# Kernel tuning notes

Measured on AMD Instinct MI355X. Metric: run time of the kernel, lower is better.

## Reference

```python
import jax, jax.numpy as jnp
import numpy as np

H = 256            # hidden_size
S = 4              # num_of_steps
B = 512            # reactions
N_MOLS = B * S     # 2048 molecules
ATOMS_PER_MOL = 32
N_ATOMS = N_MOLS * ATOMS_PER_MOL   # 65536
BONDS_PER_MOL = 64
N_BONDS = N_MOLS * BONDS_PER_MOL   # 131072 directed bonds (+1 pad row)
MAX_NB = 6
ATOM_FDIM = 133
BOND_FDIM = 147
DEPTH = 3
N_ITERS = 3  # Set2Set iterations


def setup_inputs() -> dict:
    key = jax.random.key(0)
    ks = jax.random.split(key, 20)
    def p(k, shape):
        return jax.random.normal(k, shape, jnp.float32) * 0.02
    inp = {}
    inp['f_atoms'] = jax.random.normal(ks[0], (N_ATOMS, ATOM_FDIM), jnp.float32)
    f_bonds = jax.random.normal(ks[1], (N_BONDS + 1, BOND_FDIM), jnp.float32)
    inp['f_bonds'] = f_bonds.at[0].set(0.0)  # chemprop zero pad row
    inp['a2b'] = jax.random.randint(ks[2], (N_ATOMS, MAX_NB), 0, N_BONDS + 1)
    inp['b2a'] = jax.random.randint(ks[3], (N_BONDS + 1,), 0, N_ATOMS)
    inp['b2revb'] = jax.random.randint(ks[4], (N_BONDS + 1,), 0, N_BONDS + 1)
    # MPN weights (bias=False for W_i/W_h as in args.bias default)
    inp['W_i'] = p(ks[5], (BOND_FDIM, H))
    inp['W_h'] = p(ks[6], (H, H))
    inp['W_o'] = p(ks[7], (ATOM_FDIM + H, H)); inp['b_o'] = jnp.zeros((H,), jnp.float32)
    # NNAttention over steps
    inp['W_nn0'] = p(ks[8], (2 * H, H));  inp['b_nn0'] = jnp.zeros((H,), jnp.float32)
    inp['W_nn0s'] = p(ks[9], (H, H));     inp['b_nn0s'] = jnp.zeros((H,), jnp.float32)
    inp['W_nn1'] = p(ks[10], (S * H, H)); inp['b_nn1'] = jnp.zeros((H,), jnp.float32)
    # node Set2Set (LSTM: input 2H -> hidden H) + condenser
    inp['lstm_n_Wih'] = p(ks[11], (4 * H, 2 * H))
    inp['lstm_n_Whh'] = p(ks[12], (4 * H, H))
    inp['lstm_n_b'] = jnp.zeros((4 * H,), jnp.float32)
    inp['node_cond_W'] = p(ks[13], (2 * H, H)); inp['node_cond_b'] = jnp.zeros((H,), jnp.float32)
    # graph (step) Set2Set + condenser
    inp['lstm_g_Wih'] = p(ks[14], (4 * H, 2 * H))
    inp['lstm_g_Whh'] = p(ks[15], (4 * H, H))
    inp['lstm_g_b'] = jnp.zeros((4 * H,), jnp.float32)
    inp['graph_cond_W'] = p(ks[16], (2 * H, H)); inp['graph_cond_b'] = jnp.zeros((H,), jnp.float32)
    return inp


def set2set(feat, Wih, Whh, b):
    # feat: [M, N, D]; LSTM n_layers=1, PyTorch gate order i,f,g,o
    M, N, D = feat.shape
    h = jnp.zeros((M, D), feat.dtype)
    c = jnp.zeros((M, D), feat.dtype)
    q_star = jnp.zeros((M, 2 * D), feat.dtype)
    for _ in range(N_ITERS):
        gates = q_star @ Wih.T + h @ Whh.T + b
        i, f, g, o = jnp.split(gates, 4, axis=-1)
        c = jax.nn.sigmoid(f) * c + jax.nn.sigmoid(i) * jnp.tanh(g)
        h = jax.nn.sigmoid(o) * jnp.tanh(c)
        q = h
        alpha = jax.nn.softmax(jnp.einsum('md,mnd->mn', q, feat), axis=1)
        readout = jnp.einsum('mn,mnd->md', alpha, feat)
        q_star = jnp.concatenate([q, readout], axis=-1)
    return q_star


def nn_attention(h, W0, b0, W0s, b0s, W1, b1):
    # vectorized form of the Attention module's s1/s2 double loop
    Bm, Sm, D = h.shape
    h1 = jnp.broadcast_to(h[:, :, None, :], (Bm, Sm, Sm, D))
    h2 = jnp.broadcast_to(h[:, None, :, :], (Bm, Sm, Sm, D))
    pair = jnp.concatenate([h1, h2], -1) @ W0 + b0          # [B,S,S,D] NN0(cat(h_s1,h_s2))
    self_o = h @ W0s + b0s                                   # [B,S,D]   NN0_self(h_s1)
    diag = jnp.eye(Sm, dtype=bool)[None, :, :, None]
    out = jnp.where(diag, self_o[:, :, None, :], pair)       # diagonal uses NN0_self
    return out.reshape(Bm, Sm, Sm * D) @ W1 + b1             # NN1 over s2-concat


def reference(f_atoms, f_bonds, a2b, b2a, b2revb, W_i, W_h, W_o, b_o,
              W_nn0, b_nn0, W_nn0s, b_nn0s, W_nn1, b_nn1,
              lstm_n_Wih, lstm_n_Whh, lstm_n_b, node_cond_W, node_cond_b,
              lstm_g_Wih, lstm_g_Whh, lstm_g_b, graph_cond_W, graph_cond_b):
    # --- bond message passing (chemprop, atom_messages=False) ---
    inp = f_bonds @ W_i                       # [NB+1, H], row 0 = 0 (no bias)
    message = jax.nn.relu(inp)
    message = message.at[0].set(0.0)          # keep pad row zero
    for _ in range(DEPTH - 1):
        a_message = message[a2b].sum(axis=1)          # gather+sum: [NA, H]
        msg = a_message[b2a] - message[b2revb]        # [NB+1, H]
        message = jax.nn.relu(inp + msg @ W_h)
        message = message.at[0].set(0.0)
    nei = message[a2b].sum(axis=1)                    # [NA, H]
    atom_h = jax.nn.relu(jnp.concatenate([f_atoms, nei], -1) @ W_o + b_o)
    # --- node readout: Set2Set per molecule + condenser ---
    feat = atom_h.reshape(N_MOLS, ATOMS_PER_MOL, H)
    mol = set2set(feat, lstm_n_Wih, lstm_n_Whh, lstm_n_b) @ node_cond_W + node_cond_b
    # --- step attention (NNAttention over num_of_steps) ---
    steps = mol.reshape(B, S, H)
    steps = nn_attention(steps, W_nn0, b_nn0, W_nn0s, b_nn0s, W_nn1, b_nn1)
    # --- step readout: Set2Set over steps + condenser ---
    out = set2set(steps, lstm_g_Wih, lstm_g_Whh, lstm_g_b) @ graph_cond_W + graph_cond_b
    return out  # [B, H]
```

## Files before the change

kernel.cpp:

```cpp
#include <hip/hip_runtime.h>
#include <math.h>

#define H 256
#define S_STEPS 4
#define B_RXN 512
#define N_MOLS 2048
#define ATOMS_PER_MOL 32
#define N_ATOMS 65536
#define N_BONDS 131072
#define NBP1 131073
#define MAX_NB 6
#define ATOM_FDIM 133
#define BOND_FDIM 147
#define DEPTH 3
#define N_ITERS 3

typedef unsigned short bf16u;
typedef __attribute__((ext_vector_type(8))) short short8v;
typedef __attribute__((ext_vector_type(4))) float f32x4;

__device__ __forceinline__ float b2f(bf16u u) {
    union { unsigned int i; float f; } c; c.i = ((unsigned int)u) << 16; return c.f;
}
__device__ __forceinline__ bf16u f2b(float f) {
    union { float f; unsigned int i; } c; c.f = f;
    unsigned int i = c.i;
    return (bf16u)((i + 0x7FFFu + ((i >> 16) & 1u)) >> 16);
}
__device__ __forceinline__ unsigned int relu2bf(unsigned int w) {
    unsigned int lo = w & 0xFFFFu, hi = w >> 16;
    if (lo & 0x8000u) lo = 0u;
    if (hi & 0x8000u) hi = 0u;
    return lo | (hi << 16);
}

template<int MODE, bool RELUA>
__global__ __launch_bounds__(512) void dense_gemm_k(
    const bf16u* __restrict__ A1,
    const bf16u* __restrict__ A2,
    const bf16u* __restrict__ WT,
    const float* __restrict__ bias,
    bf16u* __restrict__ outb,
    int M)
{
    constexpr int KP = (MODE == 0) ? 160 : ((MODE == 1) ? 256 : 416);
    __shared__ bf16u As[128][40];
    __shared__ bf16u Bs[256][40];

    const int tid = threadIdx.x;
    const int lane = tid & 63, w = tid >> 6;
    const int wr = w >> 2, wc = w & 3;
    const int m0 = blockIdx.x * 128;
    const int ar = tid >> 2, q8 = (tid & 3) * 8;
    const int br = tid >> 1, bh = (tid & 1) * 16;
    const int arow = m0 + ar;
    const bool rok = arow < M;
    const int lr = lane & 15, lk = (lane >> 4) * 8;
    const uint4 z4 = {0u, 0u, 0u, 0u};

    f32x4 acc[4][4];
    const f32x4 zf = {0.f, 0.f, 0.f, 0.f};
    #pragma unroll
    for (int i = 0; i < 4; ++i)
        #pragma unroll
        for (int j = 0; j < 4; ++j) acc[i][j] = zf;

    for (int k0 = 0; k0 < KP; k0 += 32) {
        const int kc = k0 + q8;
        uint4 va;
        if (MODE == 2) {
            va = (kc < 160) ? *(const uint4*)(A1 + (size_t)arow * 160 + kc)
                            : *(const uint4*)(A2 + (size_t)arow * 256 + (kc - 160));
        } else {
            constexpr int LDA = (MODE == 0) ? 160 : 256;
            va = rok ? *(const uint4*)(A1 + (size_t)arow * LDA + kc) : z4;
        }
        if (RELUA) {
            va.x = relu2bf(va.x); va.y = relu2bf(va.y);
            va.z = relu2bf(va.z); va.w = relu2bf(va.w);
        }
        *(uint4*)&As[ar][q8] = va;
        {
            const bf16u* bp = WT + (size_t)br * KP + k0 + bh;
            uint4 b0 = *(const uint4*)(bp);
            uint4 b1 = *(const uint4*)(bp + 8);
            *(uint4*)&Bs[br][bh] = b0;
            *(uint4*)&Bs[br][bh + 8] = b1;
        }
        __syncthreads();

        short8v a[4], b[4];
        #pragma unroll
        for (int mf = 0; mf < 4; ++mf)
            a[mf] = *(const short8v*)&As[wr * 64 + mf * 16 + lr][lk];
        #pragma unroll
        for (int nf = 0; nf < 4; ++nf)
            b[nf] = *(const short8v*)&Bs[wc * 64 + nf * 16 + lr][lk];
        #pragma unroll
        for (int mf = 0; mf < 4; ++mf)
            #pragma unroll
            for (int nf = 0; nf < 4; ++nf)
                acc[mf][nf] = __builtin_amdgcn_mfma_f32_16x16x32_bf16(
                    a[mf], b[nf], acc[mf][nf], 0, 0, 0);
        __syncthreads();
    }

    const int rbase = (lane >> 4) * 4;
    #pragma unroll
    for (int mf = 0; mf < 4; ++mf) {
        #pragma unroll
        for (int nf = 0; nf < 4; ++nf) {
            const int col = wc * 64 + nf * 16 + lr;
            #pragma unroll
            for (int r = 0; r < 4; ++r) {
                const int row = m0 + wr * 64 + mf * 16 + rbase + r;
                if (row >= M) continue;
                float v = acc[mf][nf][r];
                const size_t off = (size_t)row * H + col;
                if (MODE == 2) {
                    v += bias[col];
                    outb[off] = f2b(fmaxf(v, 0.f));
                } else {
                    outb[off] = f2b(v);
                }
            }
        }
    }
}

__global__ __launch_bounds__(256) void combine_k(
    const bf16u* __restrict__ inp, const bf16u* __restrict__ AP,
    const bf16u* __restrict__ MW,
    const int* __restrict__ b2a, const int* __restrict__ b2revb,
    bf16u* __restrict__ msg)
{
    int idx = blockIdx.x * 256 + threadIdx.x;
    if (idx >= NBP1 * 32) return;
    int b = idx >> 5, c = (idx & 31) * 8;
    bf16u* op = msg + (size_t)b * H + c;
    if (b == 0) {
        *(uint4*)op = make_uint4(0u, 0u, 0u, 0u);
        return;
    }
    int a = b2a[b], rb = b2revb[b];
    uint4 ui = *(const uint4*)(inp + (size_t)b * H + c);
    uint4 up = *(const uint4*)(AP + (size_t)a * H + c);
    uint4 um = *(const uint4*)(MW + (size_t)rb * H + c);
    uint4 o;
    unsigned int* pi = &ui.x; unsigned int* pp = &up.x;
    unsigned int* pm = &um.x; unsigned int* po = &o.x;
    #pragma unroll
    for (int t = 0; t < 4; ++t) {
        float lo = b2f((bf16u)(pi[t] & 0xFFFFu)) + b2f((bf16u)(pp[t] & 0xFFFFu))
                 - b2f((bf16u)(pm[t] & 0xFFFFu));
        float hi = b2f((bf16u)(pi[t] >> 16)) + b2f((bf16u)(pp[t] >> 16))
                 - b2f((bf16u)(pm[t] >> 16));
        lo = fmaxf(lo, 0.f); hi = fmaxf(hi, 0.f);
        po[t] = (unsigned int)f2b(lo) | ((unsigned int)f2b(hi) << 16);
    }
    *(uint4*)op = o;
}

template<bool BIAS>
__global__ __launch_bounds__(256) void lin64_k(
    const float* __restrict__ A1, int lda1, int KA1,
    const float* __restrict__ A2, int lda2,
    const bf16u* __restrict__ WT, int ldw,
    const float* __restrict__ bias,
    float* __restrict__ C, int ldc, int K)
{
    __shared__ bf16u As[64][40];
    __shared__ bf16u Bs[64][40];
    const int tid = threadIdx.x;
    const int lane = tid & 63, w = tid >> 6;
    const int m0 = blockIdx.x * 64;
    const int col0 = blockIdx.y * 64;
    const int ar = tid >> 2, kq8 = (tid & 3) * 8;
    const int lr = lane & 15, lk = (lane >> 4) * 8;

    f32x4 acc[4];
    const f32x4 zf = {0.f, 0.f, 0.f, 0.f};
    #pragma unroll
    for (int j = 0; j < 4; ++j) acc[j] = zf;

    for (int k0 = 0; k0 < K; k0 += 32) {
        const float* src = (k0 < KA1)
            ? (A1 + (size_t)(m0 + ar) * lda1 + k0 + kq8)
            : (A2 + (size_t)(m0 + ar) * lda2 + (k0 - KA1) + kq8);
        float4 f0 = *(const float4*)src;
        float4 f1 = *(const float4*)(src + 4);
        ushort4 s0, s1;
        s0.x = f2b(f0.x); s0.y = f2b(f0.y); s0.z = f2b(f0.z); s0.w = f2b(f0.w);
        s1.x = f2b(f1.x); s1.y = f2b(f1.y); s1.z = f2b(f1.z); s1.w = f2b(f1.w);
        *(ushort4*)&As[ar][kq8] = s0;
        *(ushort4*)&As[ar][kq8 + 4] = s1;
        *(uint4*)&Bs[ar][kq8] = *(const uint4*)(WT + (size_t)(col0 + ar) * ldw + k0 + kq8);
        __syncthreads();

        short8v a = *(const short8v*)&As[w * 16 + lr][lk];
        short8v b[4];
        #pragma unroll
        for (int nf = 0; nf < 4; ++nf)
            b[nf] = *(const short8v*)&Bs[nf * 16 + lr][lk];
        #pragma unroll
        for (int nf = 0; nf < 4; ++nf)
            acc[nf] = __builtin_amdgcn_mfma_f32_16x16x32_bf16(a, b[nf], acc[nf], 0, 0, 0);
        __syncthreads();
    }

    const int rbase = (lane >> 4) * 4;
    #pragma unroll
    for (int nf = 0; nf < 4; ++nf) {
        const int col = col0 + nf * 16 + lr;
        #pragma unroll
        for (int r = 0; r < 4; ++r) {
            const int row = m0 + w * 16 + rbase + r;
            float v = acc[nf][r];
            if (BIAS) v += bias[col];
            C[(size_t)row * ldc + col] = v;
        }
    }
}

__device__ __forceinline__ float sigm(float x) { return 1.f / (1.f + expf(-x)); }

__global__ __launch_bounds__(256) void gates_lstm_k(
    const float* __restrict__ QSTAR,
    const float* __restrict__ Hc,
    const float* __restrict__ Cc,
    const bf16u* __restrict__ WT,
    const float* __restrict__ bias,
    float* __restrict__ Hn,
    float* __restrict__ Cn,
    int M)
{
    __shared__ bf16u As[64][40];
    __shared__ bf16u Bs[64][40];
    const int tid = threadIdx.x;
    const int lane = tid & 63, w = tid >> 6;
    const int m0 = blockIdx.x * 64;
    const int db = blockIdx.y;
    const int ar = tid >> 2, q8 = (tid & 3) * 8;
    const int lr = lane & 15, lk = (lane >> 4) * 8;

    f32x4 acc[4];
    const f32x4 zf = {0.f, 0.f, 0.f, 0.f};
    #pragma unroll
    for (int g = 0; g < 4; ++g) acc[g] = zf;

    for (int k0 = 0; k0 < 768; k0 += 32) {
        const float* src = (k0 < 512)
            ? QSTAR + (size_t)(m0 + ar) * 512 + k0 + q8
            : Hc + (size_t)(m0 + ar) * 256 + (k0 - 512) + q8;
        float4 f0 = *(const float4*)src;
        float4 f1 = *(const float4*)(src + 4);
        ushort4 s0, s1;
        s0.x = f2b(f0.x); s0.y = f2b(f0.y); s0.z = f2b(f0.z); s0.w = f2b(f0.w);
        s1.x = f2b(f1.x); s1.y = f2b(f1.y); s1.z = f2b(f1.z); s1.w = f2b(f1.w);
        *(ushort4*)&As[ar][q8] = s0;
        *(ushort4*)&As[ar][q8 + 4] = s1;
        {
            int rho = tid >> 2;
            int g = rho >> 4, cn = rho & 15;
            *(uint4*)&Bs[rho][q8] =
                *(const uint4*)(WT + (size_t)(g * 256 + db * 16 + cn) * 768 + k0 + q8);
        }
        __syncthreads();
        short8v a = *(const short8v*)&As[w * 16 + lr][lk];
        #pragma unroll
        for (int g = 0; g < 4; ++g) {
            short8v b = *(const short8v*)&Bs[g * 16 + lr][lk];
            acc[g] = __builtin_amdgcn_mfma_f32_16x16x32_bf16(a, b, acc[g], 0, 0, 0);
        }
        __syncthreads();
    }

    const int rbase = (lane >> 4) * 4;
    const int d = db * 16 + lr;
    const float bi = bias[d], bf = bias[256 + d], bg = bias[512 + d], bo = bias[768 + d];
    #pragma unroll
    for (int r = 0; r < 4; ++r) {
        const int row = m0 + w * 16 + rbase + r;
        float i_ = acc[0][r] + bi;
        float f_ = acc[1][r] + bf;
        float g_ = acc[2][r] + bg;
        float o_ = acc[3][r] + bo;
        float cv = sigm(f_) * Cc[(size_t)row * 256 + d] + sigm(i_) * tanhf(g_);
        Cn[(size_t)row * 256 + d] = cv;
        Hn[(size_t)row * 256 + d] = sigm(o_) * tanhf(cv);
    }
}

__global__ __launch_bounds__(256) void lstm0_bcast_k(const float* __restrict__ bias,
                                                     float* __restrict__ Hn,
                                                     float* __restrict__ Cn, int M)
{
    int idx = blockIdx.x * 256 + threadIdx.x;
    if (idx >= M * 256) return;
    int d = idx & 255;
    float c0 = sigm(bias[d]) * tanhf(bias[512 + d]);
    float h0 = sigm(bias[768 + d]) * tanhf(c0);
    Cn[idx] = c0;
    Hn[idx] = h0;
}

__global__ __launch_bounds__(256) void prep_wt_k(const float* __restrict__ W,
                                                 bf16u* __restrict__ WT, int K, int KP)
{
    int idx = blockIdx.x * 256 + threadIdx.x;
    if (idx >= 256 * KP) return;
    int n = idx / KP, k = idx - n * KP;
    WT[idx] = (k < K) ? f2b(W[(size_t)k * H + n]) : (bf16u)0;
}

__global__ __launch_bounds__(256) void prep_wto_k(const float* __restrict__ Wo,
                                                  bf16u* __restrict__ WT)
{
    int idx = blockIdx.x * 256 + threadIdx.x;
    if (idx >= 256 * 416) return;
    int n = idx / 416, k = idx - n * 416;
    float v = 0.f;
    if (k < ATOM_FDIM) v = Wo[(size_t)k * H + n];
    else if (k >= 160) v = Wo[(size_t)(ATOM_FDIM + k - 160) * H + n];
    WT[idx] = f2b(v);
}

#define SZ_WTG   786432
#define SZ_WTNC  131072
#define SZ_WTPQS 196608
#define SZ_WTN1  262144
#define SZ_WTGC  131072
__global__ __launch_bounds__(256) void prep_mid_k(
    const float* __restrict__ Wih_n, const float* __restrict__ Whh_n,
    const float* __restrict__ Wih_g, const float* __restrict__ Whh_g,
    const float* __restrict__ ncW,  const float* __restrict__ Wnn0,
    const float* __restrict__ Wnn0s, const float* __restrict__ Wnn1,
    const float* __restrict__ gcW,  const float* __restrict__ b_nn0s,
    bf16u* __restrict__ WTG_N, bf16u* __restrict__ WTG_G,
    bf16u* __restrict__ WT_NC, bf16u* __restrict__ WT_PQS,
    bf16u* __restrict__ WT_N1, bf16u* __restrict__ WT_GC,
    float* __restrict__ BIAS_PQS)
{
    int idx = blockIdx.x * 256 + threadIdx.x;
    if (idx < SZ_WTG) {
        int n = idx / 768, k = idx - n * 768;
        WTG_N[idx] = f2b(k < 512 ? Wih_n[(size_t)n * 512 + k] : Whh_n[(size_t)n * 256 + (k - 512)]);
        return;
    }
    idx -= SZ_WTG;
    if (idx < SZ_WTG) {
        int n = idx / 768, k = idx - n * 768;
        WTG_G[idx] = f2b(k < 512 ? Wih_g[(size_t)n * 512 + k] : Whh_g[(size_t)n * 256 + (k - 512)]);
        return;
    }
    idx -= SZ_WTG;
    if (idx < SZ_WTNC) {
        int n = idx / 512, k = idx - n * 512;
        WT_NC[idx] = f2b(ncW[(size_t)k * 256 + n]);
        return;
    }
    idx -= SZ_WTNC;
    if (idx < SZ_WTPQS) {
        int n = idx / 256, k = idx - n * 256;
        float v;
        if (n < 256)      v = Wnn0[(size_t)k * 256 + n];
        else if (n < 512) v = Wnn0[(size_t)(256 + k) * 256 + (n - 256)];
        else              v = Wnn0s[(size_t)k * 256 + (n - 512)];
        WT_PQS[idx] = f2b(v);
        return;
    }
    idx -= SZ_WTPQS;
    if (idx < SZ_WTN1) {
        int n = idx / 1024, k = idx - n * 1024;
        WT_N1[idx] = f2b(Wnn1[(size_t)k * 256 + n]);
        return;
    }
    idx -= SZ_WTN1;
    if (idx < SZ_WTGC) {
        int n = idx / 512, k = idx - n * 512;
        WT_GC[idx] = f2b(gcW[(size_t)k * 256 + n]);
        return;
    }
    idx -= SZ_WTGC;
    if (idx < 768) BIAS_PQS[idx] = (idx < 512) ? 0.f : b_nn0s[idx - 512];
}
#define PREP_MID_TOTAL (2 * SZ_WTG + SZ_WTNC + SZ_WTPQS + SZ_WTN1 + SZ_WTGC + 768)

__global__ __launch_bounds__(256) void prep_feat16_k(const float* __restrict__ F,
                                                     bf16u* __restrict__ O,
                                                     int rows, int K)
{
    int idx = blockIdx.x * 256 + threadIdx.x;
    if (idx >= rows * 160) return;
    int r = idx / 160, c = idx - r * 160;
    O[idx] = (c < K) ? f2b(F[(size_t)r * K + c]) : (bf16u)0;
}

__global__ __launch_bounds__(256) void gather6_bf16_k(const bf16u* __restrict__ msg,
                                                      const int* __restrict__ a2b,
                                                      bf16u* __restrict__ outb)
{
    int idx = blockIdx.x * 256 + threadIdx.x;
    if (idx >= N_ATOMS * (H / 8)) return;
    int na = idx >> 5, c = idx & 31;
    const int* nb = a2b + (size_t)na * MAX_NB;
    float s[8] = {0.f, 0.f, 0.f, 0.f, 0.f, 0.f, 0.f, 0.f};
    #pragma unroll
    for (int j = 0; j < MAX_NB; ++j) {
        uint4 u = *(const uint4*)(msg + (size_t)nb[j] * H + c * 8);
        s[0] += b2f((bf16u)(u.x & 0xFFFFu)); s[1] += b2f((bf16u)(u.x >> 16));
        s[2] += b2f((bf16u)(u.y & 0xFFFFu)); s[3] += b2f((bf16u)(u.y >> 16));
        s[4] += b2f((bf16u)(u.z & 0xFFFFu)); s[5] += b2f((bf16u)(u.z >> 16));
        s[6] += b2f((bf16u)(u.w & 0xFFFFu)); s[7] += b2f((bf16u)(u.w >> 16));
    }
    uint4 o;
    o.x = (unsigned int)f2b(s[0]) | ((unsigned int)f2b(s[1]) << 16);
    o.y = (unsigned int)f2b(s[2]) | ((unsigned int)f2b(s[3]) << 16);
    o.z = (unsigned int)f2b(s[4]) | ((unsigned int)f2b(s[5]) << 16);
    o.w = (unsigned int)f2b(s[6]) | ((unsigned int)f2b(s[7]) << 16);
    *(uint4*)(outb + (size_t)na * H + c * 8) = o;
}

template<bool BF16F>
__global__ __launch_bounds__(256) void s2s_attn_k(const void* __restrict__ featv,
                                                  const float* __restrict__ h,
                                                  float* __restrict__ q_star, int Nn)
{
    int m = blockIdx.x;
    int t = threadIdx.x;
    int lane = t & 63, wave = t >> 6;
    __shared__ float sc[32];
    const bf16u* fb = (const bf16u*)featv;
    const float* ff = (const float*)featv;
    const size_t fbase = (size_t)m * Nn * H;
    const float* hm = h + (size_t)m * H;
    for (int n = wave; n < Nn; n += 4) {
        float p = 0.f;
        if (BF16F) {
            ushort4 u = *(const ushort4*)(fb + fbase + (size_t)n * H + lane * 4);
            const float4 h4 = *(const float4*)(hm + lane * 4);
            p = b2f(u.x) * h4.x + b2f(u.y) * h4.y + b2f(u.z) * h4.z + b2f(u.w) * h4.w;
        } else {
            const float* fr = ff + fbase + (size_t)n * H;
            #pragma unroll
            for (int u = 0; u < 4; ++u) p += fr[lane * 4 + u] * hm[lane * 4 + u];
        }
        #pragma unroll
        for (int o = 32; o >= 1; o >>= 1) p += __shfl_xor(p, o);
        if (lane == 0) sc[n] = p;
    }
    __syncthreads();
    float mx = -1e30f;
    for (int n = 0; n < Nn; ++n) mx = fmaxf(mx, sc[n]);
    float ssum = 0.f, r = 0.f;
    for (int n = 0; n < Nn; ++n) {
        float a = expf(sc[n] - mx);
        ssum += a;
        float fv = BF16F ? b2f(fb[fbase + (size_t)n * H + t]) : ff[fbase + (size_t)n * H + t];
        r += a * fv;
    }
    r /= ssum;
    q_star[(size_t)m * (2 * H) + t] = hm[t];
    q_star[(size_t)m * (2 * H) + H + t] = r;
}

__global__ __launch_bounds__(256) void build_x_k(const float* __restrict__ PQS,
                                                 const float* __restrict__ b0,
                                                 float* __restrict__ X)
{
    int idx = blockIdx.x * 256 + threadIdx.x;
    if (idx >= B_RXN * S_STEPS * S_STEPS * H) return;
    int d  = idx & 255;
    int s2 = (idx >> 8) & 3;
    int s1 = (idx >> 10) & 3;
    int b  = idx >> 12;
    float v;
    if (s1 == s2) v = PQS[((size_t)(b * S_STEPS + s1)) * 768 + 512 + d];
    else v = PQS[((size_t)(b * S_STEPS + s1)) * 768 + d]
           + PQS[((size_t)(b * S_STEPS + s2)) * 768 + 256 + d] + b0[d];
    X[idx] = v;
}

extern "C" void kernel_launch(void* const* d_in, const int* in_sizes, int n_in,
                              void* d_out, int out_size, void* d_ws, size_t ws_size,
                              hipStream_t stream)
{
    const float* f_atoms   = (const float*)d_in[0];
    const float* f_bonds   = (const float*)d_in[1];
    const int*   a2b       = (const int*)d_in[2];
    const int*   b2a       = (const int*)d_in[3];
    const int*   b2revb    = (const int*)d_in[4];
    const float* W_i       = (const float*)d_in[5];
    const float* W_h       = (const float*)d_in[6];
    const float* W_o       = (const float*)d_in[7];
    const float* b_o       = (const float*)d_in[8];
    const float* W_nn0     = (const float*)d_in[9];
    const float* b_nn0     = (const float*)d_in[10];
    const float* W_nn0s    = (const float*)d_in[11];
    const float* b_nn0s    = (const float*)d_in[12];
    const float* W_nn1     = (const float*)d_in[13];
    const float* b_nn1     = (const float*)d_in[14];
    const float* lstm_n_Wih = (const float*)d_in[15];
    const float* lstm_n_Whh = (const float*)d_in[16];
    const float* lstm_n_b   = (const float*)d_in[17];
    const float* node_cond_W = (const float*)d_in[18];
    const float* node_cond_b = (const float*)d_in[19];
    const float* lstm_g_Wih = (const float*)d_in[20];
    const float* lstm_g_Whh = (const float*)d_in[21];
    const float* lstm_g_b   = (const float*)d_in[22];
    const float* graph_cond_W = (const float*)d_in[23];
    const float* graph_cond_b = (const float*)d_in[24];
    float* out = (float*)d_out;

    const size_t SZB = (size_t)NBP1 * H * sizeof(bf16u);
    char* base = (char*)d_ws;
    bf16u* INP  = (bf16u*)(base);
    bf16u* MSG  = (bf16u*)(base + SZB);
    bf16u* MW   = (bf16u*)(base + 2 * SZB);
    bf16u* AMSG = (bf16u*)(base + 3 * SZB);
    bf16u* WT_I = (bf16u*)(base + 3 * SZB + 33554432);
    bf16u* WT_H = (bf16u*)(base + 3 * SZB + 33636352);
    bf16u* WT_O = (bf16u*)(base + 3 * SZB + 33767424);
    bf16u* FB16 = MW;
    bf16u* FA16 = MW;
    bf16u* ATOMH16 = (bf16u*)(base);
    float* SMALL = (float*)(base + SZB);
    float* HN     = SMALL + 2097152;
    float* CN     = SMALL + 2621440;
    float* QSTARN = SMALL + 3145728;
    float* MOL    = SMALL + 4194304;
    float* PQS    = SMALL + 4718592;
    float* XBUF   = SMALL + 6291456;
    float* STEPS  = SMALL + 8388608;
    float* HG     = SMALL + 8912896;
    float* CG     = SMALL + 9043968;
    float* QSTARG = SMALL + 9175040;
    float* HN2    = SMALL + 10485760;
    float* CN2    = SMALL + 11010048;
    float* HG2    = SMALL + 11534336;
    float* CG2    = SMALL + 11665408;
    char* sm2 = base + 2 * SZB + 25165824;
    bf16u* WTG_N   = (bf16u*)(sm2);
    bf16u* WTG_G   = (bf16u*)(sm2 + 1572864);
    bf16u* WT_NC   = (bf16u*)(sm2 + 3145728);
    bf16u* WT_PQS  = (bf16u*)(sm2 + 3407872);
    bf16u* WT_N1   = (bf16u*)(sm2 + 3801088);
    bf16u* WT_GC   = (bf16u*)(sm2 + 4325376);
    float* BIAS_PQS = (float*)(sm2 + 4587520);

    dim3 blk(256), blk5(512);
    const int MB_BOND = (NBP1 + 127) / 128;
    const int MB_ATOM = N_ATOMS / 128;
    const int G_GATH = (N_ATOMS * (H / 8) + 255) / 256;
    const int G_COMB = (NBP1 * 32 + 255) / 256;

    prep_wt_k<<<(256 * 160 + 255) / 256, blk, 0, stream>>>(W_i, WT_I, BOND_FDIM, 160);
    prep_wt_k<<<(256 * 256 + 255) / 256, blk, 0, stream>>>(W_h, WT_H, H, 256);
    prep_wto_k<<<(256 * 416 + 255) / 256, blk, 0, stream>>>(W_o, WT_O);
    prep_feat16_k<<<(int)(((size_t)NBP1 * 160 + 255) / 256), blk, 0, stream>>>(
        f_bonds, FB16, NBP1, BOND_FDIM);

    dense_gemm_k<0, false><<<MB_BOND, blk5, 0, stream>>>(
        FB16, nullptr, WT_I, nullptr, INP, NBP1);

    dense_gemm_k<1, true><<<MB_BOND, blk5, 0, stream>>>(
        INP, nullptr, WT_H, nullptr, MW, NBP1);
    gather6_bf16_k<<<G_GATH, blk, 0, stream>>>(MW, a2b, AMSG);
    combine_k<<<G_COMB, blk, 0, stream>>>(INP, AMSG, MW, b2a, b2revb, MSG);
    dense_gemm_k<1, false><<<MB_BOND, blk5, 0, stream>>>(
        MSG, nullptr, WT_H, nullptr, MW, NBP1);
    gather6_bf16_k<<<G_GATH, blk, 0, stream>>>(MW, a2b, AMSG);
    combine_k<<<G_COMB, blk, 0, stream>>>(INP, AMSG, MW, b2a, b2revb, MSG);

    gather6_bf16_k<<<G_GATH, blk, 0, stream>>>(MSG, a2b, AMSG);

    prep_feat16_k<<<(N_ATOMS * 160 + 255) / 256, blk, 0, stream>>>(
        f_atoms, FA16, N_ATOMS, ATOM_FDIM);
    prep_mid_k<<<(PREP_MID_TOTAL + 255) / 256, blk, 0, stream>>>(
        lstm_n_Wih, lstm_n_Whh, lstm_g_Wih, lstm_g_Whh,
        node_cond_W, W_nn0, W_nn0s, W_nn1, graph_cond_W, b_nn0s,
        WTG_N, WTG_G, WT_NC, WT_PQS, WT_N1, WT_GC, BIAS_PQS);

    dense_gemm_k<2, false><<<MB_ATOM, blk5, 0, stream>>>(
        FA16, AMSG, WT_O, b_o, ATOMH16, N_ATOMS);

    {
        lstm0_bcast_k<<<(N_MOLS * H + 255) / 256, blk, 0, stream>>>(lstm_n_b, HN, CN, N_MOLS);
        s2s_attn_k<true><<<N_MOLS, blk, 0, stream>>>(ATOMH16, HN, QSTARN, ATOMS_PER_MOL);
        float *hc = HN, *cc = CN, *hn = HN2, *cn = CN2;
        for (int it = 1; it < N_ITERS; ++it) {
            gates_lstm_k<<<dim3(N_MOLS / 64, 16), blk, 0, stream>>>(
                QSTARN, hc, cc, WTG_N, lstm_n_b, hn, cn, N_MOLS);
            s2s_attn_k<true><<<N_MOLS, blk, 0, stream>>>(ATOMH16, hn, QSTARN, ATOMS_PER_MOL);
            float* t;
            t = hc; hc = hn; hn = t;
            t = cc; cc = cn; cn = t;
        }
    }
    lin64_k<true><<<dim3(N_MOLS / 64, 4), blk, 0, stream>>>(
        QSTARN, 2 * H, 2 * H, QSTARN, 2 * H, WT_NC, 2 * H, node_cond_b, MOL, H, 2 * H);

    lin64_k<true><<<dim3(N_MOLS / 64, 12), blk, 0, stream>>>(
        MOL, H, H, MOL, H, WT_PQS, H, BIAS_PQS, PQS, 3 * H, H);
    build_x_k<<<(B_RXN * 16 * H) / 256, blk, 0, stream>>>(PQS, b_nn0, XBUF);
    lin64_k<true><<<dim3(N_MOLS / 64, 4), blk, 0, stream>>>(
        XBUF, S_STEPS * H, S_STEPS * H, XBUF, S_STEPS * H, WT_N1, S_STEPS * H, b_nn1,
        STEPS, H, S_STEPS * H);

    {
        lstm0_bcast_k<<<(B_RXN * H + 255) / 256, blk, 0, stream>>>(lstm_g_b, HG, CG, B_RXN);
        s2s_attn_k<false><<<B_RXN, blk, 0, stream>>>(STEPS, HG, QSTARG, S_STEPS);
        float *hc = HG, *cc = CG, *hn = HG2, *cn = CG2;
        for (int it = 1; it < N_ITERS; ++it) {
            gates_lstm_k<<<dim3(B_RXN / 64, 16), blk, 0, stream>>>(
                QSTARG, hc, cc, WTG_G, lstm_g_b, hn, cn, B_RXN);
            s2s_attn_k<false><<<B_RXN, blk, 0, stream>>>(STEPS, hn, QSTARG, S_STEPS);
            float* t;
            t = hc; hc = hn; hn = t;
            t = cc; cc = cn; cn = t;
        }
    }

    lin64_k<true><<<dim3(B_RXN / 64, 4), blk, 0, stream>>>(
        QSTARG, 2 * H, 2 * H, QSTARG, 2 * H, WT_GC, 2 * H, graph_cond_b, out, H, 2 * H);
}
```

Baseline: 611.7 us.

## Enlarge dense GEMM row tile to 256 and vectorize bf16 feature conversion

The dense bf16 MFMA GEMM now handles 256 rows per block instead of 128. Each warp computes a 64x128 output sub-tile with 32 accumulators, so each staged weight tile is reused across more rows, block count halves, and the global weight reads go down. The feature-to-bf16 prep kernel now converts four columns per thread and writes them with one ushort4 store. The trade-off is higher register pressure (128 accumulator floats per lane) and larger shared memory, which may cut occupancy. The last block now covers more padding rows, and in MODE 2 the A loads are not row-guarded, which only works because N_ATOMS is a multiple of 256.

```diff
diff --git a/kernel.cpp b/kernel.cpp
--- a/kernel.cpp
+++ b/kernel.cpp
@@ -44,42 +44,51 @@
     int M)
 {
     constexpr int KP = (MODE == 0) ? 160 : ((MODE == 1) ? 256 : 416);
-    __shared__ bf16u As[128][40];
+    __shared__ bf16u As[256][40];
     __shared__ bf16u Bs[256][40];
 
     const int tid = threadIdx.x;
     const int lane = tid & 63, w = tid >> 6;
-    const int wr = w >> 2, wc = w & 3;
-    const int m0 = blockIdx.x * 128;
-    const int ar = tid >> 2, q8 = (tid & 3) * 8;
+    const int wr = w & 3, wc = w >> 2;
+    const int m0 = blockIdx.x * 256;
+    const int ar = tid >> 1, q16 = (tid & 1) * 16;
     const int br = tid >> 1, bh = (tid & 1) * 16;
     const int arow = m0 + ar;
     const bool rok = arow < M;
     const int lr = lane & 15, lk = (lane >> 4) * 8;
     const uint4 z4 = {0u, 0u, 0u, 0u};
 
-    f32x4 acc[4][4];
+    f32x4 acc[4][8];
     const f32x4 zf = {0.f, 0.f, 0.f, 0.f};
     #pragma unroll
     for (int i = 0; i < 4; ++i)
         #pragma unroll
-        for (int j = 0; j < 4; ++j) acc[i][j] = zf;
+        for (int j = 0; j < 8; ++j) acc[i][j] = zf;
 
     for (int k0 = 0; k0 < KP; k0 += 32) {
-        const int kc = k0 + q8;
-        uint4 va;
+        const int kc = k0 + q16;
+        uint4 va0, va1;
         if (MODE == 2) {
-            va = (kc < 160) ? *(const uint4*)(A1 + (size_t)arow * 160 + kc)
-                            : *(const uint4*)(A2 + (size_t)arow * 256 + (kc - 160));
+            const bf16u* p = (kc < 160) ? (A1 + (size_t)arow * 160 + kc)
+                                        : (A2 + (size_t)arow * 256 + (kc - 160));
+            va0 = *(const uint4*)p;
+            va1 = *(const uint4*)(p + 8);
         } else {
             constexpr int LDA = (MODE == 0) ? 160 : 256;
-            va = rok ? *(const uint4*)(A1 + (size_t)arow * LDA + kc) : z4;
+            if (rok) {
+                const bf16u* p = A1 + (size_t)arow * LDA + kc;
+                va0 = *(const uint4*)p;
+                va1 = *(const uint4*)(p + 8);
+            } else { va0 = z4; va1 = z4; }
         }
         if (RELUA) {
-            va.x = relu2bf(va.x); va.y = relu2bf(va.y);
-            va.z = relu2bf(va.z); va.w = relu2bf(va.w);
-        }
-        *(uint4*)&As[ar][q8] = va;
+            va0.x = relu2bf(va0.x); va0.y = relu2bf(va0.y);
+            va0.z = relu2bf(va0.z); va0.w = relu2bf(va0.w);
+            va1.x = relu2bf(va1.x); va1.y = relu2bf(va1.y);
+            va1.z = relu2bf(va1.z); va1.w = relu2bf(va1.w);
+        }
+        *(uint4*)&As[ar][q16] = va0;
+        *(uint4*)&As[ar][q16 + 8] = va1;
         {
             const bf16u* bp = WT + (size_t)br * KP + k0 + bh;
             uint4 b0 = *(const uint4*)(bp);
@@ -89,17 +98,17 @@
         }
         __syncthreads();
 
-        short8v a[4], b[4];
+        short8v a[4], b[8];
         #pragma unroll
         for (int mf = 0; mf < 4; ++mf)
             a[mf] = *(const short8v*)&As[wr * 64 + mf * 16 + lr][lk];
         #pragma unroll
-        for (int nf = 0; nf < 4; ++nf)
-            b[nf] = *(const short8v*)&Bs[wc * 64 + nf * 16 + lr][lk];
+        for (int nf = 0; nf < 8; ++nf)
+            b[nf] = *(const short8v*)&Bs[wc * 128 + nf * 16 + lr][lk];
         #pragma unroll
         for (int mf = 0; mf < 4; ++mf)
             #pragma unroll
-            for (int nf = 0; nf < 4; ++nf)
+            for (int nf = 0; nf < 8; ++nf)
                 acc[mf][nf] = __builtin_amdgcn_mfma_f32_16x16x32_bf16(
                     a[mf], b[nf], acc[mf][nf], 0, 0, 0);
         __syncthreads();
@@ -109,8 +118,8 @@
     #pragma unroll
     for (int mf = 0; mf < 4; ++mf) {
         #pragma unroll
-        for (int nf = 0; nf < 4; ++nf) {
-            const int col = wc * 64 + nf * 16 + lr;
+        for (int nf = 0; nf < 8; ++nf) {
+            const int col = wc * 128 + nf * 16 + lr;
             #pragma unroll
             for (int r = 0; r < 4; ++r) {
                 const int row = m0 + wr * 64 + mf * 16 + rbase + r;
@@ -391,9 +400,15 @@
                                                      int rows, int K)
 {
     int idx = blockIdx.x * 256 + threadIdx.x;
-    if (idx >= rows * 160) return;
-    int r = idx / 160, c = idx - r * 160;
-    O[idx] = (c < K) ? f2b(F[(size_t)r * K + c]) : (bf16u)0;
+    if (idx >= rows * 40) return;
+    int r = idx / 40, c4 = (idx - r * 40) * 4;
+    const float* src = F + (size_t)r * K + c4;
+    ushort4 o;
+    o.x = (c4 + 0 < K) ? f2b(src[0]) : (bf16u)0;
+    o.y = (c4 + 1 < K) ? f2b(src[1]) : (bf16u)0;
+    o.z = (c4 + 2 < K) ? f2b(src[2]) : (bf16u)0;
+    o.w = (c4 + 3 < K) ? f2b(src[3]) : (bf16u)0;
+    *(ushort4*)(O + (size_t)r * 160 + c4) = o;
 }
 
 __global__ __launch_bounds__(256) void gather6_bf16_k(const bf16u* __restrict__ msg,
@@ -549,15 +564,15 @@
     float* BIAS_PQS = (float*)(sm2 + 4587520);
 
     dim3 blk(256), blk5(512);
-    const int MB_BOND = (NBP1 + 127) / 128;
-    const int MB_ATOM = N_ATOMS / 128;
+    const int MB_BOND = (NBP1 + 255) / 256;
+    const int MB_ATOM = N_ATOMS / 256;
     const int G_GATH = (N_ATOMS * (H / 8) + 255) / 256;
     const int G_COMB = (NBP1 * 32 + 255) / 256;
 
     prep_wt_k<<<(256 * 160 + 255) / 256, blk, 0, stream>>>(W_i, WT_I, BOND_FDIM, 160);
     prep_wt_k<<<(256 * 256 + 255) / 256, blk, 0, stream>>>(W_h, WT_H, H, 256);
     prep_wto_k<<<(256 * 416 + 255) / 256, blk, 0, stream>>>(W_o, WT_O);
-    prep_feat16_k<<<(int)(((size_t)NBP1 * 160 + 255) / 256), blk, 0, stream>>>(
+    prep_feat16_k<<<(int)(((size_t)NBP1 * 40 + 255) / 256), blk, 0, stream>>>(
         f_bonds, FB16, NBP1, BOND_FDIM);
 
     dense_gemm_k<0, false><<<MB_BOND, blk5, 0, stream>>>(
@@ -574,7 +589,7 @@
 
     gather6_bf16_k<<<G_GATH, blk, 0, stream>>>(MSG, a2b, AMSG);
 
-    prep_feat16_k<<<(N_ATOMS * 160 + 255) / 256, blk, 0, stream>>>(
+    prep_feat16_k<<<(N_ATOMS * 40 + 255) / 256, blk, 0, stream>>>(
         f_atoms, FA16, N_ATOMS, ATOM_FDIM);
     prep_mid_k<<<(PREP_MID_TOTAL + 255) / 256, blk, 0, stream>>>(
         lstm_n_Wih, lstm_n_Whh, lstm_g_Wih, lstm_g_Whh,
```

After: 635.2 us. +3.8%, slower.
